# Performance work log

Hardware: AMD Instinct MI355X
Metric: run time of the kernel (lower is better)

Reference implementation:

```python
import jax, jax.numpy as jnp
import numpy as np

BATCH, TIMESTEPS, DIM, OUT = 64, 512, 1024, 1024


def setup_inputs() -> dict:
    key = jax.random.key(0)
    k1, k2, k3, k4, k5, k6 = jax.random.split(key, 6)
    # glorot-normal-ish scales for params
    def glorot(k, shape):
        fan_in, fan_out = shape[0], shape[-1]
        std = (2.0 / (fan_in + fan_out)) ** 0.5
        return jax.random.normal(k, shape, dtype=jnp.float32) * std
    return {
        "inputs": jax.random.normal(k1, (BATCH, TIMESTEPS, DIM), dtype=jnp.float32),
        "prev_state": jax.random.normal(k2, (BATCH, OUT), dtype=jnp.float32),
        "Wa": glorot(k3, (OUT, OUT)),
        "Ua": glorot(k4, (DIM, OUT)),
        "Va": glorot(k5, (OUT, 1)),
        "Ba": glorot(k6, (1, OUT)),
    }


def reference(inputs, prev_state, Wa, Ua, Va, Ba):
    # WaS: [B, 1, OUT] broadcast over timesteps
    WaS = jnp.einsum("bo,op->bp", prev_state, Wa)[:, None, :]
    # UaH: [B, T, OUT]
    UaH = jnp.einsum("btd,do->bto", inputs, Ua)
    scores = jnp.tanh(UaH + WaS + Ba)            # [B, T, OUT]
    scores = jax.nn.relu(scores @ Va)            # [B, T, 1]
    sm = jax.nn.softmax(scores, axis=1)          # softmax over timesteps
    context_vector = jnp.sum(inputs * sm, axis=1)  # [B, DIM]
    return context_vector
```

## Files before the change

### kernel.cpp

```cpp
#include <hip/hip_runtime.h>


typedef _Float16 h8 __attribute__((ext_vector_type(8)));
typedef float f16v __attribute__((ext_vector_type(16)));

__device__ __forceinline__ float tanh_fast(float x) {
    float e = __expf(2.0f * x);
    return 1.0f - 2.0f * __builtin_amdgcn_rcpf(e + 1.0f);
}

__global__ __launch_bounds__(256) void k_pack_ua(const float* __restrict__ Ua,
                                                 _Float16* __restrict__ B16) {
    int t = blockIdx.x * 256 + threadIdx.x;
    int nn = t & 31, kg = (t >> 5) & 1, ks = (t >> 6) & 63, nt = t >> 12;
    int n = (nt << 5) + nn;
    int kbase = (ks << 4) + (kg << 3);
    h8 v;
#pragma unroll
    for (int j = 0; j < 8; ++j) v[j] = (_Float16)Ua[(size_t)(kbase + j) * 1024 + n];
    *(h8*)(B16 + ((size_t)t << 3)) = v;
}

__global__ __launch_bounds__(256) void k_pack_a(const float* __restrict__ inputs,
                                                _Float16* __restrict__ A16) {
    int w = blockIdx.x * 4 + (threadIdx.x >> 6);
    int lane = threadIdx.x & 63;
    int rb = w >> 6, ks = w & 63;
    int row = (rb << 5) + (lane & 31);
    int k = (ks << 4) + ((lane >> 5) << 3);
    const float4* src = (const float4*)(inputs + ((size_t)row << 10) + k);
    float4 v0 = src[0], v1 = src[1];
    h8 o = { (_Float16)v0.x, (_Float16)v0.y, (_Float16)v0.z, (_Float16)v0.w,
             (_Float16)v1.x, (_Float16)v1.y, (_Float16)v1.z, (_Float16)v1.w };
    *(h8*)(A16 + (((size_t)w << 6) + lane) * 8) = o;
}

__global__ __launch_bounds__(256) void k_was_part(const float* __restrict__ ps,
                                                  const float* __restrict__ Wa,
                                                  float* __restrict__ part) {
    int ic = blockIdx.x >> 2, psl = blockIdx.x & 3;
    int tid = threadIdx.x, wv = tid >> 6, lane = tid & 63;
    int p4 = psl * 64 + lane;
    const float4* Wa4 = (const float4*)Wa;
    float4* part4 = (float4*)part;
#pragma unroll 1
    for (int c = 0; c < 4; ++c) {
        int o0 = ic * 128 + c * 32;
        float4 w[32];
#pragma unroll
        for (int o = 0; o < 32; ++o) w[o] = Wa4[(size_t)(o0 + o) * 256 + p4];
#pragma unroll 1
        for (int bb = 0; bb < 16; ++bb) {
            int b = wv * 16 + bb;
            const float* psb = ps + b * 1024 + o0;
            size_t oidx = (size_t)((ic << 6) + b) * 256 + p4;
            float4 a;
            if (c == 0) { a.x = a.y = a.z = a.w = 0.f; }
            else        { a = part4[oidx]; }
#pragma unroll
            for (int o = 0; o < 32; ++o) {
                float s = psb[o];
                a.x += s * w[o].x; a.y += s * w[o].y;
                a.z += s * w[o].z; a.w += s * w[o].w;
            }
            part4[oidx] = a;
        }
    }
}

__global__ __launch_bounds__(256) void k_was_reduce(const float* __restrict__ part,
                                                    const float* __restrict__ Ba,
                                                    float* __restrict__ wsWaS) {
    int b = blockIdx.x, tid = threadIdx.x;
    const float4* p4 = (const float4*)part;
    float4 acc = ((const float4*)Ba)[tid];
#pragma unroll
    for (int ic = 0; ic < 8; ++ic) {
        float4 v = p4[((ic << 6) + b) * 256 + tid];
        acc.x += v.x; acc.y += v.y; acc.z += v.z; acc.w += v.w;
    }
    ((float4*)wsWaS)[b * 256 + tid] = acc;
}

__global__ __launch_bounds__(256, 2) void k_fused_gemm(
    const _Float16* __restrict__ A16, const _Float16* __restrict__ B16,
    const float* __restrict__ wsWaS, const float* __restrict__ Va,
    float* __restrict__ scores)
{
    __shared__ float scoreSh[64];
    const int tid = threadIdx.x;
    const int lane = tid & 63, wv = tid >> 6;
    const int l31 = lane & 31, lhi = lane >> 5;
    const int r0 = blockIdx.x * 64;
    const int rb0 = blockIdx.x * 2;
    const int b = r0 >> 9;

    if (tid < 64) scoreSh[tid] = 0.0f;
    __syncthreads();

    const h8* A8 = (const h8*)A16;
    const h8* B8 = (const h8*)B16;
    const h8* aBase = A8 + ((size_t)rb0 << 12) + lane;

    for (int pass = 0; pass < 2; ++pass) {
        const int ntb = (pass << 4) + (wv << 2);
        const h8* bBase = B8 + ((size_t)ntb << 12) + lane;

        f16v acc[2][4];
#pragma unroll
        for (int rt = 0; rt < 2; ++rt)
#pragma unroll
            for (int ct = 0; ct < 4; ++ct)
#pragma unroll
                for (int e = 0; e < 16; ++e) acc[rt][ct][e] = 0.0f;

        h8 af[2][2], bf[2][4];
#pragma unroll
        for (int rt = 0; rt < 2; ++rt) af[0][rt] = aBase[rt * 4096];
#pragma unroll
        for (int ct = 0; ct < 4; ++ct) bf[0][ct] = bBase[ct * 4096];

#pragma unroll 4
        for (int ks = 0; ks < 64; ++ks) {
            const int cur = ks & 1, nxt = cur ^ 1;
            if (ks < 63) {
                const int o = (ks + 1) << 6;
#pragma unroll
                for (int rt = 0; rt < 2; ++rt) af[nxt][rt] = aBase[rt * 4096 + o];
#pragma unroll
                for (int ct = 0; ct < 4; ++ct) bf[nxt][ct] = bBase[ct * 4096 + o];
            }
#pragma unroll
            for (int rt = 0; rt < 2; ++rt)
#pragma unroll
                for (int ct = 0; ct < 4; ++ct)
                    acc[rt][ct] = __builtin_amdgcn_mfma_f32_32x32x16_f16(
                        af[cur][rt], bf[cur][ct], acc[rt][ct], 0, 0, 0);
        }

        float wsv[4], vav[4];
#pragma unroll
        for (int ct = 0; ct < 4; ++ct) {
            int n = (ntb + ct) << 5 | l31;
            wsv[ct] = wsWaS[b * 1024 + n];
            vav[ct] = Va[n];
        }
#pragma unroll
        for (int rt = 0; rt < 2; ++rt) {
#pragma unroll
            for (int i = 0; i < 16; ++i) {
                float s = 0.0f;
#pragma unroll
                for (int ct = 0; ct < 4; ++ct)
                    s += tanh_fast(acc[rt][ct][i] + wsv[ct]) * vav[ct];
                s += __shfl_xor(s, 1);
                s += __shfl_xor(s, 2);
                s += __shfl_xor(s, 4);
                s += __shfl_xor(s, 8);
                s += __shfl_xor(s, 16);
                if (l31 == 0) {
                    int row = rt * 32 + (i & 3) + ((i >> 2) << 3) + (lhi << 2);
                    atomicAdd(&scoreSh[row], s);
                }
            }
        }
    }
    __syncthreads();
    if (tid < 64) scores[r0 + tid] = fmaxf(scoreSh[tid], 0.0f);
}

__global__ __launch_bounds__(256) void k_softmax(const float* __restrict__ scores,
                                                 float* __restrict__ sm) {
    int b = blockIdx.x, tid = threadIdx.x;
    __shared__ float red[256];
    const float* sb = scores + b * 512;
    float s0 = sb[tid], s1 = sb[tid + 256];
    red[tid] = fmaxf(s0, s1);
    __syncthreads();
    for (int st = 128; st > 0; st >>= 1) {
        if (tid < st) red[tid] = fmaxf(red[tid], red[tid + st]);
        __syncthreads();
    }
    float m = red[0];
    __syncthreads();
    float e0 = __expf(s0 - m), e1 = __expf(s1 - m);
    red[tid] = e0 + e1;
    __syncthreads();
    for (int st = 128; st > 0; st >>= 1) {
        if (tid < st) red[tid] += red[tid + st];
        __syncthreads();
    }
    float inv = 1.0f / red[0];
    sm[b * 512 + tid] = e0 * inv;
    sm[b * 512 + 256 + tid] = e1 * inv;
}

__global__ __launch_bounds__(256) void k_ctx_part(const float* __restrict__ inputs,
                                                  const float* __restrict__ sm,
                                                  float* __restrict__ part) {
    int ts = blockIdx.x, b = blockIdx.y, tid = threadIdx.x;
    const float4* inF4 = (const float4*)inputs;
    float4 acc = {0.f, 0.f, 0.f, 0.f};
    int t0 = ts * 64;
#pragma unroll 8
    for (int t = t0; t < t0 + 64; ++t) {
        float wgt = sm[b * 512 + t];
        float4 x = inF4[(size_t)(b * 512 + t) * 256 + tid];
        acc.x += wgt * x.x; acc.y += wgt * x.y; acc.z += wgt * x.z; acc.w += wgt * x.w;
    }
    ((float4*)part)[((ts << 6) + b) * 256 + tid] = acc;
}

__global__ __launch_bounds__(256) void k_ctx_reduce(const float* __restrict__ part,
                                                    float* __restrict__ out) {
    int g = blockIdx.x * 256 + threadIdx.x;
    const float4* p4 = (const float4*)part;
    float4 acc = p4[g];
#pragma unroll
    for (int s = 1; s < 8; ++s) {
        float4 v = p4[s * 16384 + g];
        acc.x += v.x; acc.y += v.y; acc.z += v.z; acc.w += v.w;
    }
    ((float4*)out)[g] = acc;
}

extern "C" void kernel_launch(void* const* d_in, const int* in_sizes, int n_in,
                              void* d_out, int out_size, void* d_ws, size_t ws_size,
                              hipStream_t stream) {
    const float* inputs = (const float*)d_in[0];
    const float* prev   = (const float*)d_in[1];
    const float* Wa     = (const float*)d_in[2];
    const float* Ua     = (const float*)d_in[3];
    const float* Va     = (const float*)d_in[4];
    const float* Ba     = (const float*)d_in[5];
    float* out = (float*)d_out;

    char* ws = (char*)d_ws;
    _Float16* A16   = (_Float16*)(ws);
    _Float16* B16   = (_Float16*)(ws + (64u << 20));
    float* wasPart  = (float*)(ws + (66u << 20));
    float* wsWaS    = (float*)(ws + (68u << 20));
    float* scores   = (float*)(ws + (68u << 20) + (256u << 10));
    float* sm       = (float*)(ws + (68u << 20) + (384u << 10));
    float* ctxPart  = (float*)(ws + (68u << 20) + (512u << 10));

    hipLaunchKernelGGL(k_pack_ua,    dim3(512),    dim3(256), 0, stream, Ua, B16);
    hipLaunchKernelGGL(k_pack_a,     dim3(16384),  dim3(256), 0, stream, inputs, A16);
    hipLaunchKernelGGL(k_was_part,   dim3(32),     dim3(256), 0, stream, prev, Wa, wasPart);
    hipLaunchKernelGGL(k_was_reduce, dim3(64),     dim3(256), 0, stream, wasPart, Ba, wsWaS);
    hipLaunchKernelGGL(k_fused_gemm, dim3(512),    dim3(256), 0, stream, A16, B16, wsWaS, Va, scores);
    hipLaunchKernelGGL(k_softmax,    dim3(64),     dim3(256), 0, stream, scores, sm);
    hipLaunchKernelGGL(k_ctx_part,   dim3(8, 64),  dim3(256), 0, stream, inputs, sm, ctxPart);
    hipLaunchKernelGGL(k_ctx_reduce, dim3(64),     dim3(256), 0, stream, ctxPart, out);
}
```

Baseline: 377.9 us.

## Read fp16 packed inputs for context sum, deepen A prefetch, restructure pack_a

The context-vector stage now reads the fp16 packed A16 buffer instead of the fp32 inputs, halving that traffic. It also reduces across timesteps within each wave via shuffles, which drops the partial-sum buffer and the separate reduce kernel. The pack_a kernel is restructured so each thread converts 16 chunks per block with fewer blocks, and the GEMM prefetches A fragments four k-steps ahead instead of one. The trade-off is fp16 rounding of inputs in the final weighted sum, which changes accuracy relative to the fp32 reference.

```diff
diff --git a/kernel.cpp b/kernel.cpp
--- a/kernel.cpp
+++ b/kernel.cpp
@@ -23,16 +23,18 @@
 
 __global__ __launch_bounds__(256) void k_pack_a(const float* __restrict__ inputs,
                                                 _Float16* __restrict__ A16) {
-    int w = blockIdx.x * 4 + (threadIdx.x >> 6);
-    int lane = threadIdx.x & 63;
-    int rb = w >> 6, ks = w & 63;
-    int row = (rb << 5) + (lane & 31);
-    int k = (ks << 4) + ((lane >> 5) << 3);
-    const float4* src = (const float4*)(inputs + ((size_t)row << 10) + k);
-    float4 v0 = src[0], v1 = src[1];
-    h8 o = { (_Float16)v0.x, (_Float16)v0.y, (_Float16)v0.z, (_Float16)v0.w,
-             (_Float16)v1.x, (_Float16)v1.y, (_Float16)v1.z, (_Float16)v1.w };
-    *(h8*)(A16 + (((size_t)w << 6) + lane) * 8) = o;
+    const int bx = blockIdx.x, t = threadIdx.x;
+    const int rl = t >> 3, oc0 = t & 7;
+    const float4* src = (const float4*)(inputs + (((size_t)bx * 32 + rl) << 10));
+    h8* dst = (h8*)A16 + ((size_t)bx << 12) + rl;
+#pragma unroll
+    for (int i = 0; i < 16; ++i) {
+        int o = oc0 + (i << 3);
+        float4 v0 = src[o * 2], v1 = src[o * 2 + 1];
+        h8 ov = { (_Float16)v0.x, (_Float16)v0.y, (_Float16)v0.z, (_Float16)v0.w,
+                  (_Float16)v1.x, (_Float16)v1.y, (_Float16)v1.z, (_Float16)v1.w };
+        dst[((o >> 1) << 6) + ((o & 1) << 5)] = ov;
+    }
 }
 
 __global__ __launch_bounds__(256) void k_was_part(const float* __restrict__ ps,
@@ -114,28 +116,33 @@
 #pragma unroll
                 for (int e = 0; e < 16; ++e) acc[rt][ct][e] = 0.0f;
 
-        h8 af[2][2], bf[2][4];
-#pragma unroll
-        for (int rt = 0; rt < 2; ++rt) af[0][rt] = aBase[rt * 4096];
+        h8 af[4][2], bf[2][4];
+#pragma unroll
+        for (int p = 0; p < 4; ++p)
+#pragma unroll
+            for (int rt = 0; rt < 2; ++rt) af[p][rt] = aBase[rt * 4096 + p * 64];
 #pragma unroll
         for (int ct = 0; ct < 4; ++ct) bf[0][ct] = bBase[ct * 4096];
 
 #pragma unroll 4
         for (int ks = 0; ks < 64; ++ks) {
-            const int cur = ks & 1, nxt = cur ^ 1;
+            const int cur = ks & 1, nxt = cur ^ 1, ra = ks & 3;
+            h8 a0 = af[ra][0], a1 = af[ra][1];
+            if (ks < 60) {
+                const int o = (ks + 4) << 6;
+                af[ra][0] = aBase[o];
+                af[ra][1] = aBase[4096 + o];
+            }
             if (ks < 63) {
                 const int o = (ks + 1) << 6;
 #pragma unroll
-                for (int rt = 0; rt < 2; ++rt) af[nxt][rt] = aBase[rt * 4096 + o];
-#pragma unroll
                 for (int ct = 0; ct < 4; ++ct) bf[nxt][ct] = bBase[ct * 4096 + o];
             }
 #pragma unroll
-            for (int rt = 0; rt < 2; ++rt)
-#pragma unroll
-                for (int ct = 0; ct < 4; ++ct)
-                    acc[rt][ct] = __builtin_amdgcn_mfma_f32_32x32x16_f16(
-                        af[cur][rt], bf[cur][ct], acc[rt][ct], 0, 0, 0);
+            for (int ct = 0; ct < 4; ++ct) {
+                acc[0][ct] = __builtin_amdgcn_mfma_f32_32x32x16_f16(a0, bf[cur][ct], acc[0][ct], 0, 0, 0);
+                acc[1][ct] = __builtin_amdgcn_mfma_f32_32x32x16_f16(a1, bf[cur][ct], acc[1][ct], 0, 0, 0);
+            }
         }
 
         float wsv[4], vav[4];
@@ -195,33 +202,35 @@
     sm[b * 512 + 256 + tid] = e1 * inv;
 }
 
-__global__ __launch_bounds__(256) void k_ctx_part(const float* __restrict__ inputs,
-                                                  const float* __restrict__ sm,
-                                                  float* __restrict__ part) {
-    int ts = blockIdx.x, b = blockIdx.y, tid = threadIdx.x;
-    const float4* inF4 = (const float4*)inputs;
-    float4 acc = {0.f, 0.f, 0.f, 0.f};
-    int t0 = ts * 64;
-#pragma unroll 8
-    for (int t = t0; t < t0 + 64; ++t) {
-        float wgt = sm[b * 512 + t];
-        float4 x = inF4[(size_t)(b * 512 + t) * 256 + tid];
-        acc.x += wgt * x.x; acc.y += wgt * x.y; acc.z += wgt * x.z; acc.w += wgt * x.w;
-    }
-    ((float4*)part)[((ts << 6) + b) * 256 + tid] = acc;
-}
-
-__global__ __launch_bounds__(256) void k_ctx_reduce(const float* __restrict__ part,
-                                                    float* __restrict__ out) {
-    int g = blockIdx.x * 256 + threadIdx.x;
-    const float4* p4 = (const float4*)part;
-    float4 acc = p4[g];
-#pragma unroll
-    for (int s = 1; s < 8; ++s) {
-        float4 v = p4[s * 16384 + g];
-        acc.x += v.x; acc.y += v.y; acc.z += v.z; acc.w += v.w;
-    }
-    ((float4*)out)[g] = acc;
+__global__ __launch_bounds__(256) void k_ctx(const _Float16* __restrict__ A16,
+                                             const float* __restrict__ sm,
+                                             float* __restrict__ out) {
+    const int bx = blockIdx.x, b = blockIdx.y;
+    const int tid = threadIdx.x, wv = tid >> 6, lane = tid & 63;
+    const int l31 = lane & 31, lhi = lane >> 5;
+    const h8* A8 = (const h8*)A16;
+    const int ksl = bx * 4 + wv;
+    float facc[8];
+#pragma unroll
+    for (int j = 0; j < 8; ++j) facc[j] = 0.0f;
+    const float* smb = sm + b * 512;
+#pragma unroll 4
+    for (int rbl = 0; rbl < 16; ++rbl) {
+        h8 x = A8[(((size_t)(b * 16 + rbl) << 6) + ksl) * 64 + lane];
+        float wgt = smb[rbl * 32 + l31];
+#pragma unroll
+        for (int j = 0; j < 8; ++j) facc[j] += wgt * (float)x[j];
+    }
+#pragma unroll
+    for (int m = 1; m < 32; m <<= 1)
+#pragma unroll
+        for (int j = 0; j < 8; ++j) facc[j] += __shfl_xor(facc[j], m);
+    if (l31 == 0) {
+        int oct = bx * 8 + wv * 2 + lhi;
+        float* o = out + b * 1024 + oct * 8;
+#pragma unroll
+        for (int j = 0; j < 8; ++j) o[j] = facc[j];
+    }
 }
 
 extern "C" void kernel_launch(void* const* d_in, const int* in_sizes, int n_in,
@@ -242,14 +251,12 @@
     float* wsWaS    = (float*)(ws + (68u << 20));
     float* scores   = (float*)(ws + (68u << 20) + (256u << 10));
     float* sm       = (float*)(ws + (68u << 20) + (384u << 10));
-    float* ctxPart  = (float*)(ws + (68u << 20) + (512u << 10));
 
     hipLaunchKernelGGL(k_pack_ua,    dim3(512),    dim3(256), 0, stream, Ua, B16);
-    hipLaunchKernelGGL(k_pack_a,     dim3(16384),  dim3(256), 0, stream, inputs, A16);
+    hipLaunchKernelGGL(k_pack_a,     dim3(1024),   dim3(256), 0, stream, inputs, A16);
     hipLaunchKernelGGL(k_was_part,   dim3(32),     dim3(256), 0, stream, prev, Wa, wasPart);
     hipLaunchKernelGGL(k_was_reduce, dim3(64),     dim3(256), 0, stream, wasPart, Ba, wsWaS);
     hipLaunchKernelGGL(k_fused_gemm, dim3(512),    dim3(256), 0, stream, A16, B16, wsWaS, Va, scores);
     hipLaunchKernelGGL(k_softmax,    dim3(64),     dim3(256), 0, stream, scores, sm);
-    hipLaunchKernelGGL(k_ctx_part,   dim3(8, 64),  dim3(256), 0, stream, inputs, sm, ctxPart);
-    hipLaunchKernelGGL(k_ctx_reduce, dim3(64),     dim3(256), 0, stream, ctxPart, out);
-}
+    hipLaunchKernelGGL(k_ctx,        dim3(16, 64), dim3(256), 0, stream, A16, sm, out);
+}
```

After: 367.3 us. -2.8%, faster.
